# Kernel optimization log

Hardware: AMD Instinct MI355X
Metric: run time of the kernel (lower is better)

## Reference

```python
import jax, jax.numpy as jnp
import numpy as np

FINE_RES = 128      # fine grid resolution per axis
POOL = 2            # kernel_size == stride == 2
COARSE_RES = FINE_RES // POOL  # 64


def setup_inputs() -> dict:
    key = jax.random.key(0)
    kf, kc = jax.random.split(key)
    N, C = 1000000, 64
    features = jax.random.normal(kf, (N, C), dtype=jnp.float32)
    coords = jax.random.randint(kc, (N, 3), 0, FINE_RES, dtype=jnp.int32)
    num_segments = COARSE_RES ** 3  # 262144 coarse voxels (dense linearization)
    return {"features": features, "coords": coords, "num_segments": num_segments}


def reference(features, coords, num_segments):
    # Sparse 3D max pool with kernel==stride==2: each fine voxel maps to
    # exactly one coarse voxel floor(ijk / 2); reduce by segment max.
    cc = coords // POOL  # [N,3] coarse ijk
    seg = (cc[:, 0] * COARSE_RES + cc[:, 1]) * COARSE_RES + cc[:, 2]  # [N] linear coarse id
    pooled = jax.ops.segment_max(features, seg, num_segments=num_segments)  # [S,C]
    # fvdb fills uncovered coarse voxels with -inf; module masks inf -> 0
    pooled = jnp.where(jnp.isinf(pooled), jnp.zeros((), pooled.dtype), pooled)
    return pooled
```

## Files before the change

### kernel.cpp

```cpp
#include <hip/hip_runtime.h>
#include <math.h>


#define CHANNELS 64
#define COARSE_RES 64
#define NSEG (COARSE_RES * COARSE_RES * COARSE_RES)
#define CAP 16
#define MAXOVF 65536

__global__ void scatter_kernel(const int* __restrict__ coords,
                               int* __restrict__ cursor,
                               int* __restrict__ ovf,
                               int* __restrict__ indices,
                               int n) {
    int p = blockIdx.x * blockDim.x + threadIdx.x;
    if (p >= n) return;
    int ci = coords[3 * p + 0] >> 1;
    int cj = coords[3 * p + 1] >> 1;
    int ck = coords[3 * p + 2] >> 1;
    int seg = (ci * COARSE_RES + cj) * COARSE_RES + ck;
    int pos = atomicAdd(&cursor[seg], 1);
    if (pos < CAP) {
        indices[seg * CAP + pos] = p;
    } else {
        int o = atomicAdd(&ovf[0], 1);
        if (o < MAXOVF) {
            ovf[16 + 2 * o + 0] = p;
            ovf[16 + 2 * o + 1] = seg;
        }
    }
}

__global__ void gather_max_kernel(const float* __restrict__ feat,
                                  const int* __restrict__ indices,
                                  const int* __restrict__ cursor,
                                  float* __restrict__ out) {
    int wave = (blockIdx.x * blockDim.x + threadIdx.x) >> 6;
    int lane = threadIdx.x & 63;
    int g = lane >> 4;
    int q = lane & 15;
    int cnt = cursor[wave];
    int idx = indices[wave * CAP + q];
    cnt = min(cnt, CAP);
    float4 m = make_float4(0.f, 0.f, 0.f, 0.f);
    if (cnt > 0) {
        m = make_float4(-INFINITY, -INFINITY, -INFINITY, -INFINITY);
        for (int t = 0; t * 4 < cnt; ++t) {
            int s = min(t * 4 + g, cnt - 1);
            int p = __shfl(idx, s);
            float4 f = reinterpret_cast<const float4*>(feat + (long)p * CHANNELS)[q];
            m.x = fmaxf(m.x, f.x);
            m.y = fmaxf(m.y, f.y);
            m.z = fmaxf(m.z, f.z);
            m.w = fmaxf(m.w, f.w);
        }
        m.x = fmaxf(m.x, __shfl_xor(m.x, 16));
        m.y = fmaxf(m.y, __shfl_xor(m.y, 16));
        m.z = fmaxf(m.z, __shfl_xor(m.z, 16));
        m.w = fmaxf(m.w, __shfl_xor(m.w, 16));
        m.x = fmaxf(m.x, __shfl_xor(m.x, 32));
        m.y = fmaxf(m.y, __shfl_xor(m.y, 32));
        m.z = fmaxf(m.z, __shfl_xor(m.z, 32));
        m.w = fmaxf(m.w, __shfl_xor(m.w, 32));
    }
    if (lane < 16) {
        reinterpret_cast<float4*>(out)[(long)wave * 16 + q] = m;
    }
}

__global__ void overflow_kernel(const float* __restrict__ feat,
                                const int* __restrict__ ovf,
                                float* __restrict__ out) {
    int n = min(ovf[0], MAXOVF);
    int total = n * CHANNELS;
    int stride = gridDim.x * blockDim.x;
    for (int k = blockIdx.x * blockDim.x + threadIdx.x; k < total; k += stride) {
        int e = k >> 6;
        int c = k & 63;
        int p = ovf[16 + 2 * e + 0];
        int seg = ovf[16 + 2 * e + 1];
        float v = feat[(long)p * CHANNELS + c];
        int* addr = (int*)&out[(long)seg * CHANNELS + c];
        int old = *addr;
        while (__int_as_float(old) < v) {
            int assumed = old;
            old = atomicCAS(addr, assumed, __float_as_int(v));
            if (old == assumed) break;
        }
    }
}

extern "C" void kernel_launch(void* const* d_in, const int* in_sizes, int n_in,
                              void* d_out, int out_size, void* d_ws, size_t ws_size,
                              hipStream_t stream) {
    const float* feat = (const float*)d_in[0];
    const int* coords = (const int*)d_in[1];
    int npoints = in_sizes[0] / CHANNELS;

    int* cursor  = (int*)d_ws;
    int* ovf     = cursor + NSEG;
    int* indices = ovf + 16 + 2 * MAXOVF;

    const int BLOCK = 256;

    hipMemsetAsync(cursor, 0, (NSEG + 16) * sizeof(int), stream);

    int grid_pts = (npoints + BLOCK - 1) / BLOCK;
    scatter_kernel<<<grid_pts, BLOCK, 0, stream>>>(coords, cursor, ovf, indices, npoints);

    int grid_gather = NSEG / (BLOCK / 64);
    gather_max_kernel<<<grid_gather, BLOCK, 0, stream>>>(feat, indices, cursor, (float*)d_out);

    overflow_kernel<<<16, BLOCK, 0, stream>>>(feat, ovf, (float*)d_out);
}
```

Before: 174.8 us.

## Process eight segments per wave with double-buffered software-pipelined gathers

The gather kernel now handles a strip of eight coarse segments per wave, one channel per lane, and keeps two batches of four feature-row loads in flight (double buffering) across segment boundaries, so memory latency overlaps with reduction and stores. Empty segments are written as zero directly. The hipMemsetAsync is replaced with a grid-stride zeroing kernel. The aim is to hide gather latency and cut per-segment wave overhead, at the cost of more complex control flow, divergence-prone loops and scalar instead of float4 loads.

```diff
diff --git a/kernel.cpp b/kernel.cpp
--- a/kernel.cpp
+++ b/kernel.cpp
@@ -7,6 +7,13 @@
 #define NSEG (COARSE_RES * COARSE_RES * COARSE_RES)
 #define CAP 16
 #define MAXOVF 65536
+#define SPW 8
+
+__global__ void zero_kernel(int* __restrict__ buf, int n) {
+    int i = blockIdx.x * blockDim.x + threadIdx.x;
+    int stride = gridDim.x * blockDim.x;
+    for (; i < n; i += stride) buf[i] = 0;
+}
 
 __global__ void scatter_kernel(const int* __restrict__ coords,
                                int* __restrict__ cursor,
@@ -31,41 +38,80 @@
     }
 }
 
-__global__ void gather_max_kernel(const float* __restrict__ feat,
-                                  const int* __restrict__ indices,
-                                  const int* __restrict__ cursor,
-                                  float* __restrict__ out) {
+__global__ __launch_bounds__(256) void gather_strip_kernel(
+        const float* __restrict__ feat,
+        const int* __restrict__ indices,
+        const int* __restrict__ cursor,
+        float* __restrict__ out) {
     int wave = (blockIdx.x * blockDim.x + threadIdx.x) >> 6;
     int lane = threadIdx.x & 63;
-    int g = lane >> 4;
-    int q = lane & 15;
-    int cnt = cursor[wave];
-    int idx = indices[wave * CAP + q];
-    cnt = min(cnt, CAP);
-    float4 m = make_float4(0.f, 0.f, 0.f, 0.f);
-    if (cnt > 0) {
-        m = make_float4(-INFINITY, -INFINITY, -INFINITY, -INFINITY);
-        for (int t = 0; t * 4 < cnt; ++t) {
-            int s = min(t * 4 + g, cnt - 1);
-            int p = __shfl(idx, s);
-            float4 f = reinterpret_cast<const float4*>(feat + (long)p * CHANNELS)[q];
-            m.x = fmaxf(m.x, f.x);
-            m.y = fmaxf(m.y, f.y);
-            m.z = fmaxf(m.z, f.z);
-            m.w = fmaxf(m.w, f.w);
+    long segbase = (long)wave * SPW;
+
+    int cnt_l = 0;
+    if (lane < SPW) {
+        cnt_l = cursor[segbase + lane];
+        if (cnt_l > CAP) cnt_l = CAP;
+    }
+    int2 idx2 = reinterpret_cast<const int2*>(indices + segbase * CAP)[lane];
+
+    int s = 0, t = 0, cs = 0;
+    float m = -INFINITY;
+
+    #define SKIP_EMPTIES()                                         \
+        for (;;) {                                                 \
+            if (s >= SPW) break;                                   \
+            cs = __shfl(cnt_l, s);                                 \
+            if (cs > 0) break;                                     \
+            out[(segbase + s) * CHANNELS + lane] = 0.0f;           \
+            ++s;                                                   \
         }
-        m.x = fmaxf(m.x, __shfl_xor(m.x, 16));
-        m.y = fmaxf(m.y, __shfl_xor(m.y, 16));
-        m.z = fmaxf(m.z, __shfl_xor(m.z, 16));
-        m.w = fmaxf(m.w, __shfl_xor(m.w, 16));
-        m.x = fmaxf(m.x, __shfl_xor(m.x, 32));
-        m.y = fmaxf(m.y, __shfl_xor(m.y, 32));
-        m.z = fmaxf(m.z, __shfl_xor(m.z, 32));
-        m.w = fmaxf(m.w, __shfl_xor(m.w, 32));
+
+    #define EXTRACT(r, dst) {                                      \
+        int lsrc = (s << 3) + ((r) >> 1);                          \
+        int lo_ = __shfl(idx2.x, lsrc);                            \
+        int hi_ = __shfl(idx2.y, lsrc);                            \
+        dst = ((r) & 1) ? hi_ : lo_; }
+
+    #define ISSUE(F0, F1, F2, F3, FLUSH, SEG) {                    \
+        int r0_ = t;                                               \
+        int r1_ = min(t + 1, cs - 1);                              \
+        int r2_ = min(t + 2, cs - 1);                              \
+        int r3_ = min(t + 3, cs - 1);                              \
+        int p0_, p1_, p2_, p3_;                                    \
+        EXTRACT(r0_, p0_); EXTRACT(r1_, p1_);                      \
+        EXTRACT(r2_, p2_); EXTRACT(r3_, p3_);                      \
+        F0 = feat[(long)p0_ * CHANNELS + lane];                    \
+        F1 = feat[(long)p1_ * CHANNELS + lane];                    \
+        F2 = feat[(long)p2_ * CHANNELS + lane];                    \
+        F3 = feat[(long)p3_ * CHANNELS + lane];                    \
+        t += 4;                                                    \
+        FLUSH = (t >= cs); SEG = s;                                \
+        if (FLUSH) { ++s; t = 0; SKIP_EMPTIES(); } }
+
+    #define CONSUME(F0, F1, F2, F3, FLUSH, SEG) {                  \
+        m = fmaxf(m, fmaxf(fmaxf(F0, F1), fmaxf(F2, F3)));         \
+        if (FLUSH) {                                               \
+            out[(segbase + SEG) * CHANNELS + lane] = m;            \
+            m = -INFINITY; } }
+
+    SKIP_EMPTIES();
+    float fA0, fA1, fA2, fA3, fB0, fB1, fB2, fB3;
+    bool flA = false, flB = false;
+    int sgA = 0, sgB = 0;
+    bool haveA = false, haveB = false;
+    if (s < SPW) { ISSUE(fA0, fA1, fA2, fA3, flA, sgA); haveA = true; }
+    if (s < SPW) { ISSUE(fB0, fB1, fB2, fB3, flB, sgB); haveB = true; }
+    while (haveA) {
+        CONSUME(fA0, fA1, fA2, fA3, flA, sgA); haveA = false;
+        if (s < SPW) { ISSUE(fA0, fA1, fA2, fA3, flA, sgA); haveA = true; }
+        if (!haveB) { if (!haveA) break; else continue; }
+        CONSUME(fB0, fB1, fB2, fB3, flB, sgB); haveB = false;
+        if (s < SPW) { ISSUE(fB0, fB1, fB2, fB3, flB, sgB); haveB = true; }
     }
-    if (lane < 16) {
-        reinterpret_cast<float4*>(out)[(long)wave * 16 + q] = m;
-    }
+    #undef SKIP_EMPTIES
+    #undef EXTRACT
+    #undef ISSUE
+    #undef CONSUME
 }
 
 __global__ void overflow_kernel(const float* __restrict__ feat,
@@ -103,13 +149,13 @@
 
     const int BLOCK = 256;
 
-    hipMemsetAsync(cursor, 0, (NSEG + 16) * sizeof(int), stream);
+    zero_kernel<<<512, BLOCK, 0, stream>>>(cursor, NSEG + 16);
 
     int grid_pts = (npoints + BLOCK - 1) / BLOCK;
     scatter_kernel<<<grid_pts, BLOCK, 0, stream>>>(coords, cursor, ovf, indices, npoints);
 
-    int grid_gather = NSEG / (BLOCK / 64);
-    gather_max_kernel<<<grid_gather, BLOCK, 0, stream>>>(feat, indices, cursor, (float*)d_out);
+    int grid_gather = NSEG / (SPW * (BLOCK / 64));
+    gather_strip_kernel<<<grid_gather, BLOCK, 0, stream>>>(feat, indices, cursor, (float*)d_out);
 
     overflow_kernel<<<16, BLOCK, 0, stream>>>(feat, ovf, (float*)d_out);
 }
```

After: 140.5 us. 19.6% less time.
